# Kernel optimization log

Hardware: AMD Instinct MI355X
Metric: run time of the kernel (lower is better)

## Reference

```python
import jax, jax.numpy as jnp
import numpy as np

B, N, F_IN, F_OUT = 65536, 17, 64, 64


def setup_inputs() -> dict:
    key = jax.random.key(0)
    k1, k2, k3, k4 = jax.random.split(key, 4)
    x = jax.random.normal(k1, (B, N, F_IN), dtype=jnp.float32)
    adj = jax.random.uniform(k2, (N, N), dtype=jnp.float32)
    # symmetric 0/1-ish skeleton adjacency with self structure kept dense as in the module
    adj = (adj + adj.T) * 0.5
    weight_self = jax.random.normal(k3, (F_IN, F_OUT), dtype=jnp.float32) * (1.0 / np.sqrt(F_IN))
    weight_neighbor = jax.random.normal(k4, (F_IN, F_OUT), dtype=jnp.float32) * (1.0 / np.sqrt(F_IN))
    bias = jnp.zeros((F_OUT,), dtype=jnp.float32)
    return {"x": x, "adj": adj, "weight_self": weight_self,
            "weight_neighbor": weight_neighbor, "bias": bias}


def reference(x, adj, weight_self, weight_neighbor, bias):
    # out_self[b,n,o] = x[b,n,i] * W_self[i,o]
    out_self = jnp.einsum('bni,io->bno', x, weight_self)
    # neighbor aggregation: adj[n,m] * x[b,m,i]
    x_neighbors = jnp.einsum('nm,bmi->bni', adj, x)
    out_neighbors = jnp.einsum('bni,io->bno', x_neighbors, weight_neighbor)
    return out_self + out_neighbors + bias
```

## Files before the change

### kernel.cpp

```cpp
#include <hip/hip_runtime.h>
#include <stdint.h>

#define NNODE 17
#define FDIM  64
#define GPB   8
#define ROWS  (GPB*NNODE)
#define LDK   132
#define NBLOCK 512
#define ITERS  16

typedef __attribute__((ext_vector_type(4)))  short short4v;
typedef __attribute__((ext_vector_type(8)))  short short8v;
typedef __attribute__((ext_vector_type(16))) float f32x16;

__device__ __forceinline__ uint32_t bf16b(float f) {
    uint32_t u = __float_as_uint(f);
    return (u + 0x7fffu + ((u >> 16) & 1u)) >> 16;
}
__device__ __forceinline__ uint32_t bfpack(float lo, float hi) {
    return bf16b(lo) | (bf16b(hi) << 16);
}
__device__ __forceinline__ short8v ld8(const uint16_t* p) {
    short4v lo = *(const short4v*)p;
    short4v hi = *(const short4v*)(p + 4);
    return __builtin_shufflevector(lo, hi, 0, 1, 2, 3, 4, 5, 6, 7);
}

__global__ __launch_bounds__(256, 3) void egc_kernel(
    const float* __restrict__ x, const float* __restrict__ adj,
    const float* __restrict__ wself, const float* __restrict__ wneigh,
    const float* __restrict__ bias, float* __restrict__ out)
{
    __shared__ uint16_t sXZ[160][LDK];
    __shared__ float sAdj[NNODE * NNODE];
    __shared__ float sBias[FDIM];

    const int t  = threadIdx.x;
    const int l  = t & 63;
    const int wv = t >> 6;
    const int n_ = l & 31;
    const int h_ = l >> 5;

    for (int i = t; i < 24 * LDK; i += 256) ((uint16_t*)&sXZ[136][0])[i] = 0;

    for (int idx = t; idx < FDIM * 128; idx += 256) {
        int o = idx >> 7, k = idx & 127;
        float v = (k < 64) ? wself[k * 64 + o] : wneigh[(k - 64) * 64 + o];
        sXZ[o][k] = (uint16_t)bf16b(v);
    }
    for (int i = t; i < NNODE * NNODE; i += 256) sAdj[i] = adj[i];
    if (t < FDIM) sBias[t] = bias[t];
    __syncthreads();

    const int ctw = wv & 1;
    short8v wfrag[8];
    #pragma unroll
    for (int ks = 0; ks < 8; ++ks)
        wfrag[ks] = ld8(&sXZ[32 * ctw + n_][16 * ks + 8 * h_]);
    const float breg = sBias[32 * ctw + n_];

    short8v zb[2];
    #pragma unroll
    for (int ks = 0; ks < 2; ++ks) {
        short8v v;
        #pragma unroll
        for (int e = 0; e < 8; ++e) {
            int k = 16 * ks + 8 * h_ + e;
            float a = (k < NNODE && n_ < NNODE) ? sAdj[n_ * NNODE + k] : 0.f;
            v[e] = (short)bf16b(a);
        }
        zb[ks] = v;
    }
    __syncthreads();

    float4 pf[9];
    const size_t cbase = (size_t)blockIdx.x * ITERS;
    const float4* xg0 = (const float4*)x;
    {
        const float4* xg = xg0 + cbase * (ROWS * 16);
        #pragma unroll
        for (int j = 0; j < 8; ++j) pf[j] = xg[t + j * 256];
        if (t < 128) pf[8] = xg[t + 2048];
    }

    for (int it = 0; it < ITERS; ++it) {
        #pragma unroll
        for (int j = 0; j < 9; ++j) {
            if (j < 8 || t < 128) {
                int idx = t + j * 256;
                int row = idx >> 4, c4 = (idx & 15) << 2;
                float4 v = pf[j];
                uint2 pk; pk.x = bfpack(v.x, v.y); pk.y = bfpack(v.z, v.w);
                *(uint2*)&sXZ[row][c4] = pk;
            }
        }
        __syncthreads();

        if (it + 1 < ITERS) {
            const float4* xg = xg0 + (cbase + it + 1) * (ROWS * 16);
            #pragma unroll
            for (int j = 0; j < 8; ++j) pf[j] = xg[t + j * 256];
            if (t < 128) pf[8] = xg[t + 2048];
        }

        #pragma unroll
        for (int uu = 0; uu < 4; ++uu) {
            int u = wv * 4 + uu;
            int g = u >> 1, mt = u & 1;
            f32x16 zacc;
            #pragma unroll
            for (int r = 0; r < 16; ++r) zacc[r] = 0.f;
            #pragma unroll
            for (int ks = 0; ks < 2; ++ks) {
                const uint16_t* base = &sXZ[g * NNODE + 16 * ks + 8 * h_][32 * mt + n_];
                short8v a;
                #pragma unroll
                for (int e = 0; e < 8; ++e) a[e] = (short)base[e * LDK];
                zacc = __builtin_amdgcn_mfma_f32_32x32x16_bf16(a, zb[ks], zacc, 0, 0, 0);
            }
            if (n_ < NNODE) {
                uint16_t* zrow = &sXZ[g * NNODE + n_][64 + 32 * mt + 4 * h_];
                #pragma unroll
                for (int q = 0; q < 4; ++q) {
                    uint2 pk;
                    pk.x = bfpack(zacc[4 * q + 0], zacc[4 * q + 1]);
                    pk.y = bfpack(zacc[4 * q + 2], zacc[4 * q + 3]);
                    *(uint2*)&zrow[8 * q] = pk;
                }
            }
        }
        __syncthreads();

        {
            float* outg = out + (cbase + it) * (size_t)(ROWS * FDIM);
            #pragma unroll
            for (int ri = 0; ri < 3; ++ri) {
                int rt = (wv >> 1) + 2 * ri;
                if (rt < 5) {
                    f32x16 acc;
                    #pragma unroll
                    for (int r = 0; r < 16; ++r) acc[r] = breg;
                    #pragma unroll
                    for (int ks = 0; ks < 8; ++ks) {
                        short8v a = ld8(&sXZ[32 * rt + n_][16 * ks + 8 * h_]);
                        acc = __builtin_amdgcn_mfma_f32_32x32x16_bf16(a, wfrag[ks], acc, 0, 0, 0);
                    }
                    #pragma unroll
                    for (int r = 0; r < 16; ++r) {
                        int row = 32 * rt + (r & 3) + 8 * (r >> 2) + 4 * h_;
                        if (rt < 4 || r < 4)
                            outg[row * 64 + 32 * ctw + n_] = acc[r];
                    }
                }
            }
        }
        __syncthreads();
    }
}

extern "C" void kernel_launch(void* const* d_in, const int* in_sizes, int n_in,
                              void* d_out, int out_size, void* d_ws, size_t ws_size,
                              hipStream_t stream) {
    (void)in_sizes; (void)n_in; (void)d_ws; (void)ws_size; (void)out_size;
    const float* x      = (const float*)d_in[0];
    const float* adj    = (const float*)d_in[1];
    const float* wself  = (const float*)d_in[2];
    const float* wneigh = (const float*)d_in[3];
    const float* bias   = (const float*)d_in[4];
    float* out = (float*)d_out;
    egc_kernel<<<NBLOCK, 256, 0, stream>>>(x, adj, wself, wneigh, bias, out);
}
```

Baseline: 134.1 us.

## Reassociate neighbor term as adj·(X·Wn) with per-wave graph ownership

Each wave now handles its own 32 graphs, one graph at a time, in a private LDS strip, so block-wide barriers in the main loop go away. The math is reordered to compute X·Ws and X·Wn with MFMA and then apply the adjacency to X·Wn. The intermediate is moved between lanes with shuffles instead of a round trip through LDS. This trades padded 32-row MFMA tiles for 17-node graphs, and more wasted MFMA work, plus higher register use (launch bounds 3→2), for fewer syncs and less LDS traffic.

```diff
diff --git a/kernel.cpp b/kernel.cpp
--- a/kernel.cpp
+++ b/kernel.cpp
@@ -1,13 +1,12 @@
 #include <hip/hip_runtime.h>
 #include <stdint.h>
 
-#define NNODE 17
-#define FDIM  64
-#define GPB   8
-#define ROWS  (GPB*NNODE)
-#define LDK   132
+#define NNODE  17
+#define FDIM   64
 #define NBLOCK 512
-#define ITERS  16
+#define GPW    32
+#define SROW   68
+#define WSTR   132
 
 typedef __attribute__((ext_vector_type(4)))  short short4v;
 typedef __attribute__((ext_vector_type(8)))  short short8v;
@@ -25,13 +24,18 @@
     short4v hi = *(const short4v*)(p + 4);
     return __builtin_shufflevector(lo, hi, 0, 1, 2, 3, 4, 5, 6, 7);
 }
+__device__ __forceinline__ short8v mk8(uint32_t w0, uint32_t w1, uint32_t w2, uint32_t w3) {
+    union { uint32_t u[4]; short8v v; } c;
+    c.u[0] = w0; c.u[1] = w1; c.u[2] = w2; c.u[3] = w3;
+    return c.v;
+}
 
-__global__ __launch_bounds__(256, 3) void egc_kernel(
+__global__ __launch_bounds__(256, 2) void egc_kernel(
     const float* __restrict__ x, const float* __restrict__ adj,
     const float* __restrict__ wself, const float* __restrict__ wneigh,
     const float* __restrict__ bias, float* __restrict__ out)
 {
-    __shared__ uint16_t sXZ[160][LDK];
+    __shared__ uint16_t sMem[4 * 32 * SROW];
     __shared__ float sAdj[NNODE * NNODE];
     __shared__ float sBias[FDIM];
 
@@ -41,120 +45,142 @@
     const int n_ = l & 31;
     const int h_ = l >> 5;
 
-    for (int i = t; i < 24 * LDK; i += 256) ((uint16_t*)&sXZ[136][0])[i] = 0;
+    const int    gw    = blockIdx.x * 4 + wv;
+    const size_t gbase = (size_t)gw * GPW;
+
+    const float4* xg = (const float4*)x + gbase * 272;
+    float4 pf0, pf1, pf2, pf3, pf4;
+    pf0 = xg[l]; pf1 = xg[l + 64]; pf2 = xg[l + 128]; pf3 = xg[l + 192];
+    if (l < 16) pf4 = xg[256 + l];
 
     for (int idx = t; idx < FDIM * 128; idx += 256) {
         int o = idx >> 7, k = idx & 127;
         float v = (k < 64) ? wself[k * 64 + o] : wneigh[(k - 64) * 64 + o];
-        sXZ[o][k] = (uint16_t)bf16b(v);
+        sMem[o * WSTR + k] = (uint16_t)bf16b(v);
     }
     for (int i = t; i < NNODE * NNODE; i += 256) sAdj[i] = adj[i];
     if (t < FDIM) sBias[t] = bias[t];
     __syncthreads();
 
-    const int ctw = wv & 1;
-    short8v wfrag[8];
+    short8v wS[2][4], wN[2][4];
     #pragma unroll
-    for (int ks = 0; ks < 8; ++ks)
-        wfrag[ks] = ld8(&sXZ[32 * ctw + n_][16 * ks + 8 * h_]);
-    const float breg = sBias[32 * ctw + n_];
+    for (int nt = 0; nt < 2; ++nt)
+        #pragma unroll
+        for (int ks = 0; ks < 4; ++ks) {
+            wS[nt][ks] = ld8(&sMem[(32 * nt + n_) * WSTR + 16 * ks + 8 * h_]);
+            wN[nt][ks] = ld8(&sMem[(32 * nt + n_) * WSTR + 64 + 16 * ks + 8 * h_]);
+        }
+    const float bias0 = sBias[n_], bias1 = sBias[32 + n_];
 
-    short8v zb[2];
+    short8v adjA[2];
     #pragma unroll
     for (int ks = 0; ks < 2; ++ks) {
         short8v v;
         #pragma unroll
         for (int e = 0; e < 8; ++e) {
             int k = 16 * ks + 8 * h_ + e;
-            float a = (k < NNODE && n_ < NNODE) ? sAdj[n_ * NNODE + k] : 0.f;
+            float a = (n_ < NNODE && k < NNODE) ? sAdj[n_ * NNODE + k] : 0.f;
             v[e] = (short)bf16b(a);
         }
-        zb[ks] = v;
+        adjA[ks] = v;
     }
     __syncthreads();
+    for (int i = t; i < 4 * 32 * SROW; i += 256) sMem[i] = 0;
+    __syncthreads();
 
-    float4 pf[9];
-    const size_t cbase = (size_t)blockIdx.x * ITERS;
-    const float4* xg0 = (const float4*)x;
-    {
-        const float4* xg = xg0 + cbase * (ROWS * 16);
-        #pragma unroll
-        for (int j = 0; j < 8; ++j) pf[j] = xg[t + j * 256];
-        if (t < 128) pf[8] = xg[t + 2048];
-    }
+    uint16_t* strip = &sMem[wv * 32 * SROW];
+    float* outg = out + gbase * (size_t)(NNODE * FDIM);
 
-    for (int it = 0; it < ITERS; ++it) {
-        #pragma unroll
-        for (int j = 0; j < 9; ++j) {
-            if (j < 8 || t < 128) {
-                int idx = t + j * 256;
-                int row = idx >> 4, c4 = (idx & 15) << 2;
-                float4 v = pf[j];
-                uint2 pk; pk.x = bfpack(v.x, v.y); pk.y = bfpack(v.z, v.w);
-                *(uint2*)&sXZ[row][c4] = pk;
+    for (int g = 0; g < GPW; ++g) {
+        {
+            uint2 pk; int idx, row, c4;
+            idx = l;       row = idx >> 4; c4 = (idx & 15) << 2;
+            pk.x = bfpack(pf0.x, pf0.y); pk.y = bfpack(pf0.z, pf0.w);
+            *(uint2*)&strip[row * SROW + c4] = pk;
+            idx = l + 64;  row = idx >> 4; c4 = (idx & 15) << 2;
+            pk.x = bfpack(pf1.x, pf1.y); pk.y = bfpack(pf1.z, pf1.w);
+            *(uint2*)&strip[row * SROW + c4] = pk;
+            idx = l + 128; row = idx >> 4; c4 = (idx & 15) << 2;
+            pk.x = bfpack(pf2.x, pf2.y); pk.y = bfpack(pf2.z, pf2.w);
+            *(uint2*)&strip[row * SROW + c4] = pk;
+            idx = l + 192; row = idx >> 4; c4 = (idx & 15) << 2;
+            pk.x = bfpack(pf3.x, pf3.y); pk.y = bfpack(pf3.z, pf3.w);
+            *(uint2*)&strip[row * SROW + c4] = pk;
+            if (l < 16) {
+                pk.x = bfpack(pf4.x, pf4.y); pk.y = bfpack(pf4.z, pf4.w);
+                *(uint2*)&strip[16 * SROW + (l << 2)] = pk;
             }
         }
-        __syncthreads();
-
-        if (it + 1 < ITERS) {
-            const float4* xg = xg0 + (cbase + it + 1) * (ROWS * 16);
-            #pragma unroll
-            for (int j = 0; j < 8; ++j) pf[j] = xg[t + j * 256];
-            if (t < 128) pf[8] = xg[t + 2048];
+        if (g + 1 < GPW) {
+            xg += 272;
+            pf0 = xg[l]; pf1 = xg[l + 64]; pf2 = xg[l + 128]; pf3 = xg[l + 192];
+            if (l < 16) pf4 = xg[256 + l];
         }
 
+        short8v a0 = ld8(&strip[n_ * SROW + 0  + 8 * h_]);
+        short8v a1 = ld8(&strip[n_ * SROW + 16 + 8 * h_]);
+        short8v a2 = ld8(&strip[n_ * SROW + 32 + 8 * h_]);
+        short8v a3 = ld8(&strip[n_ * SROW + 48 + 8 * h_]);
+
+        f32x16 s0, s1, h0, h1;
         #pragma unroll
-        for (int uu = 0; uu < 4; ++uu) {
-            int u = wv * 4 + uu;
-            int g = u >> 1, mt = u & 1;
-            f32x16 zacc;
+        for (int r = 0; r < 16; ++r) { s0[r] = bias0; s1[r] = bias1; h0[r] = 0.f; h1[r] = 0.f; }
+
+        s0 = __builtin_amdgcn_mfma_f32_32x32x16_bf16(a0, wS[0][0], s0, 0, 0, 0);
+        s1 = __builtin_amdgcn_mfma_f32_32x32x16_bf16(a0, wS[1][0], s1, 0, 0, 0);
+        h0 = __builtin_amdgcn_mfma_f32_32x32x16_bf16(a0, wN[0][0], h0, 0, 0, 0);
+        h1 = __builtin_amdgcn_mfma_f32_32x32x16_bf16(a0, wN[1][0], h1, 0, 0, 0);
+        s0 = __builtin_amdgcn_mfma_f32_32x32x16_bf16(a1, wS[0][1], s0, 0, 0, 0);
+        s1 = __builtin_amdgcn_mfma_f32_32x32x16_bf16(a1, wS[1][1], s1, 0, 0, 0);
+        h0 = __builtin_amdgcn_mfma_f32_32x32x16_bf16(a1, wN[0][1], h0, 0, 0, 0);
+        h1 = __builtin_amdgcn_mfma_f32_32x32x16_bf16(a1, wN[1][1], h1, 0, 0, 0);
+        s0 = __builtin_amdgcn_mfma_f32_32x32x16_bf16(a2, wS[0][2], s0, 0, 0, 0);
+        s1 = __builtin_amdgcn_mfma_f32_32x32x16_bf16(a2, wS[1][2], s1, 0, 0, 0);
+        h0 = __builtin_amdgcn_mfma_f32_32x32x16_bf16(a2, wN[0][2], h0, 0, 0, 0);
+        h1 = __builtin_amdgcn_mfma_f32_32x32x16_bf16(a2, wN[1][2], h1, 0, 0, 0);
+        s0 = __builtin_amdgcn_mfma_f32_32x32x16_bf16(a3, wS[0][3], s0, 0, 0, 0);
+        s1 = __builtin_amdgcn_mfma_f32_32x32x16_bf16(a3, wS[1][3], s1, 0, 0, 0);
+        h0 = __builtin_amdgcn_mfma_f32_32x32x16_bf16(a3, wN[0][3], h0, 0, 0, 0);
+        h1 = __builtin_amdgcn_mfma_f32_32x32x16_bf16(a3, wN[1][3], h1, 0, 0, 0);
+
+        #define HB_ADJ(SACC, HACC)                                                        \
+        {                                                                                  \
+            _Pragma("unroll")                                                              \
+            for (int ks2 = 0; ks2 < 2; ++ks2) {                                            \
+                const int rb = 8 * ks2;                                                    \
+                float o0_ = __shfl_xor(h_ ? HACC[rb + 0] : HACC[rb + 4], 32);              \
+                float o1_ = __shfl_xor(h_ ? HACC[rb + 1] : HACC[rb + 5], 32);              \
+                float o2_ = __shfl_xor(h_ ? HACC[rb + 2] : HACC[rb + 6], 32);              \
+                float o3_ = __shfl_xor(h_ ? HACC[rb + 3] : HACC[rb + 7], 32);              \
+                uint32_t l01 = bfpack(HACC[rb + 0], HACC[rb + 1]);                         \
+                uint32_t l23 = bfpack(HACC[rb + 2], HACC[rb + 3]);                         \
+                uint32_t l45 = bfpack(HACC[rb + 4], HACC[rb + 5]);                         \
+                uint32_t l67 = bfpack(HACC[rb + 6], HACC[rb + 7]);                         \
+                uint32_t o01 = bfpack(o0_, o1_);                                           \
+                uint32_t o23 = bfpack(o2_, o3_);                                           \
+                uint32_t w0 = h_ ? o01 : l01;                                              \
+                uint32_t w1 = h_ ? o23 : l23;                                              \
+                uint32_t w2 = h_ ? l45 : o01;                                              \
+                uint32_t w3 = h_ ? l67 : o23;                                              \
+                SACC = __builtin_amdgcn_mfma_f32_32x32x16_bf16(                            \
+                    adjA[ks2], mk8(w0, w1, w2, w3), SACC, 0, 0, 0);                        \
+            }                                                                              \
+        }
+        HB_ADJ(s0, h0)
+        HB_ADJ(s1, h1)
+        #undef HB_ADJ
+
+        {
+            float* og = outg + (size_t)g * (NNODE * FDIM);
             #pragma unroll
-            for (int r = 0; r < 16; ++r) zacc[r] = 0.f;
-            #pragma unroll
-            for (int ks = 0; ks < 2; ++ks) {
-                const uint16_t* base = &sXZ[g * NNODE + 16 * ks + 8 * h_][32 * mt + n_];
-                short8v a;
-                #pragma unroll
-                for (int e = 0; e < 8; ++e) a[e] = (short)base[e * LDK];
-                zacc = __builtin_amdgcn_mfma_f32_32x32x16_bf16(a, zb[ks], zacc, 0, 0, 0);
-            }
-            if (n_ < NNODE) {
-                uint16_t* zrow = &sXZ[g * NNODE + n_][64 + 32 * mt + 4 * h_];
-                #pragma unroll
-                for (int q = 0; q < 4; ++q) {
-                    uint2 pk;
-                    pk.x = bfpack(zacc[4 * q + 0], zacc[4 * q + 1]);
-                    pk.y = bfpack(zacc[4 * q + 2], zacc[4 * q + 3]);
-                    *(uint2*)&zrow[8 * q] = pk;
+            for (int r = 0; r < 9; ++r) {
+                int row = (r & 3) + 8 * (r >> 2) + 4 * h_;
+                if (row < NNODE) {
+                    og[row * 64 + n_]      = s0[r];
+                    og[row * 64 + 32 + n_] = s1[r];
                 }
             }
         }
-        __syncthreads();
-
-        {
-            float* outg = out + (cbase + it) * (size_t)(ROWS * FDIM);
-            #pragma unroll
-            for (int ri = 0; ri < 3; ++ri) {
-                int rt = (wv >> 1) + 2 * ri;
-                if (rt < 5) {
-                    f32x16 acc;
-                    #pragma unroll
-                    for (int r = 0; r < 16; ++r) acc[r] = breg;
-                    #pragma unroll
-                    for (int ks = 0; ks < 8; ++ks) {
-                        short8v a = ld8(&sXZ[32 * rt + n_][16 * ks + 8 * h_]);
-                        acc = __builtin_amdgcn_mfma_f32_32x32x16_bf16(a, wfrag[ks], acc, 0, 0, 0);
-                    }
-                    #pragma unroll
-                    for (int r = 0; r < 16; ++r) {
-                        int row = 32 * rt + (r & 3) + 8 * (r >> 2) + 4 * h_;
-                        if (rt < 4 || r < 4)
-                            outg[row * 64 + 32 * ctw + n_] = acc[r];
-                    }
-                }
-            }
-        }
-        __syncthreads();
     }
 }
 
```

Result: no change. 136.5 us (+1.8%).
